# Optimization experiments

Measured on AMD Instinct MI355X. Metric: run time of the kernel, lower is better.

Reference implementation:

```python
import jax, jax.numpy as jnp
import numpy as np

B, K, Z = 16384, 4096, 64  # batch, codebook size, code dim


def _linear_params(key, fan_in, fan_out):
    kw, kb = jax.random.split(key)
    lim = 1.0 / np.sqrt(fan_in)
    W = jax.random.uniform(kw, (fan_out, fan_in), jnp.float32, -lim, lim)
    b = jax.random.uniform(kb, (fan_out,), jnp.float32, -lim, lim)
    return W, b


def setup_inputs() -> dict:
    key = jax.random.key(0)
    ks = jax.random.split(key, 10)
    X = jax.random.normal(ks[0], (B, 784), jnp.float32)
    We1, be1 = _linear_params(ks[1], 784, 1000)
    We2, be2 = _linear_params(ks[2], 1000, 500)
    We3, be3 = _linear_params(ks[3], 500, 300)
    We4, be4 = _linear_params(ks[4], 300, Z)
    emb = jax.random.normal(ks[5], (K, Z), jnp.float32)  # nn.Embedding default N(0,1)
    Wd1, bd1 = _linear_params(ks[6], Z, 300)
    Wd2, bd2 = _linear_params(ks[7], 300, 500)
    Wd3, bd3 = _linear_params(ks[8], 500, 1000)
    Wd4, bd4 = _linear_params(ks[9], 1000, 784)
    return dict(X=X, We1=We1, be1=be1, We2=We2, be2=be2, We3=We3, be3=be3,
                We4=We4, be4=be4, emb=emb, Wd1=Wd1, bd1=bd1, Wd2=Wd2, bd2=bd2,
                Wd3=Wd3, bd3=bd3, Wd4=Wd4, bd4=bd4)


def _lin(x, W, b):
    return x @ W.T + b


def _nearest(query, target):
    # squared euclidean distances [Q, T] via expanded form (same math, no QxTxZ blowup)
    q2 = jnp.sum(query * query, axis=1, keepdims=True)        # [Q,1]
    t2 = jnp.sum(target * target, axis=1)                      # [T]
    d = q2 - 2.0 * (query @ target.T) + t2[None, :]            # [Q,T]
    idx = jnp.argmin(d, axis=1)                                # first min, like torch .min
    return target[idx]


def reference(X, We1, be1, We2, be2, We3, be3, We4, be4, emb,
              Wd1, bd1, Wd2, bd2, Wd3, bd3, Wd4, bd4):
    x = X.reshape(-1, 784)
    h = jax.nn.relu(_lin(x, We1, be1))
    h = jax.nn.relu(_lin(h, We2, be2))
    h = jax.nn.relu(_lin(h, We3, be3))
    Z_enc = _lin(h, We4, be4)                                  # [B,Z]
    Z_emb = _nearest(Z_enc, emb)                               # [B,Z]
    d = jax.nn.leaky_relu(_lin(Z_emb, Wd1, bd1), 0.1)
    d = jax.nn.leaky_relu(_lin(d, Wd2, bd2), 0.1)
    d = jax.nn.leaky_relu(_lin(d, Wd3, bd3), 0.1)
    Z_dec = jnp.tanh(_lin(d, Wd4, bd4)).reshape(-1, 1, 28, 28)
    Z_enc_for_emb = _nearest(emb, Z_enc)                       # [K,Z]
    return (Z_dec, Z_enc, Z_dec, Z_enc_for_emb)
```

## Files before the change

kernel.cpp:

```cpp
#include <hip/hip_runtime.h>
#include <hip/hip_bf16.h>
#include <math.h>

typedef __bf16 bf16_t;
typedef __bf16 bf16x8 __attribute__((ext_vector_type(8)));
typedef __bf16 bf16x4 __attribute__((ext_vector_type(4)));
typedef float f32x4 __attribute__((ext_vector_type(4)));

__device__ __forceinline__ void gload16(const void* g, void* l)
{
    __builtin_amdgcn_global_load_lds(
        (const __attribute__((address_space(1))) void*)g,
        (__attribute__((address_space(3))) void*)l, 16, 0, 0);
}

template<int ACT, int CB>
__global__ __launch_bounds__(256)
void np_gemm2(const float* __restrict__ A, const float* __restrict__ W,
              const float* __restrict__ bias, float* __restrict__ C,
              int N, int Cstride, int KP, int KA, int Kreal)
{
    __shared__ __align__(16) float sA[128 * 32];
    __shared__ __align__(16) float sB[CB * 64 * 32];
    const int tid = threadIdx.x;
    const int tx  = tid & 15, ty = tid >> 4;
    const int bRow = blockIdx.x * 128, bCol = blockIdx.y * (CB * 64);

    float acc[8][CB * 4];
#pragma unroll
    for (int i = 0; i < 8; ++i)
#pragma unroll
        for (int j = 0; j < CB * 4; ++j) acc[i][j] = 0.f;

    const int aswz = ty & 7;
    const int bswz = tx & 7;

    for (int k0 = 0; k0 < KP; k0 += 32) {
        __syncthreads();
        if (k0 + 32 <= Kreal) {
#pragma unroll
            for (int i = 0; i < 4; ++i) {
                int L = tid + i * 256;
                int r = L >> 3, cc = L & 7;
                int gc = cc ^ ((r >> 2) & 7);
                gload16(A + (size_t)(bRow + r) * KA + (k0 + gc * 4), sA + L * 4);
            }
        } else {
#pragma unroll
            for (int i = 0; i < 4; ++i) {
                int L = tid + i * 256;
                int r = L >> 3, cc = L & 7;
                int gc = cc ^ ((r >> 2) & 7);
                int gk = k0 + gc * 4;
                float4 v = make_float4(0.f, 0.f, 0.f, 0.f);
                if (gk < Kreal) v = *(const float4*)(A + (size_t)(bRow + r) * KA + gk);
                *(float4*)(sA + L * 4) = v;
            }
        }
#pragma unroll
        for (int i = 0; i < CB * 2; ++i) {
            int L = tid + i * 256;
            int r = L >> 3, cc = L & 7;
            int gc = cc ^ ((r >> 2) & 7);
            gload16(W + (size_t)(bCol + r) * KP + (k0 + gc * 4), sB + L * 4);
        }
        __syncthreads();

#pragma unroll
        for (int kc = 0; kc < 8; ++kc) {
            const int ac = ((kc ^ aswz) << 2);
            const int bc = ((kc ^ bswz) << 2);
            float4 b4[CB][4];
#pragma unroll
            for (int jb = 0; jb < CB; ++jb)
#pragma unroll
                for (int j = 0; j < 4; ++j)
                    b4[jb][j] = *(const float4*)(sB + (jb * 64 + tx * 4 + j) * 32 + bc);
#pragma unroll
            for (int ib = 0; ib < 2; ++ib)
#pragma unroll
                for (int i = 0; i < 4; ++i) {
                    float4 a4 = *(const float4*)(sA + (ib * 64 + ty * 4 + i) * 32 + ac);
#pragma unroll
                    for (int jb = 0; jb < CB; ++jb)
#pragma unroll
                        for (int j = 0; j < 4; ++j) {
                            float& o = acc[ib * 4 + i][jb * 4 + j];
                            o = __fmaf_rn(a4.x, b4[jb][j].x, o);
                            o = __fmaf_rn(a4.y, b4[jb][j].y, o);
                            o = __fmaf_rn(a4.z, b4[jb][j].z, o);
                            o = __fmaf_rn(a4.w, b4[jb][j].w, o);
                        }
                }
        }
    }

#pragma unroll
    for (int jb = 0; jb < CB; ++jb) {
        int col4 = bCol + jb * 64 + tx * 4;
        if (col4 >= Cstride) continue;
#pragma unroll
        for (int ib = 0; ib < 2; ++ib)
#pragma unroll
            for (int i = 0; i < 4; ++i) {
                int row = bRow + ib * 64 + ty * 4 + i;
                float ov[4];
#pragma unroll
                for (int j = 0; j < 4; ++j) {
                    int col = col4 + j;
                    float v = 0.f;
                    if (col < N) {
                        v = __fadd_rn(acc[ib * 4 + i][jb * 4 + j], bias[col]);
                        if (ACT == 1) v = v > 0.f ? v : 0.f;
                    }
                    ov[j] = v;
                }
                *(float4*)(C + (size_t)row * Cstride + col4) =
                    make_float4(ov[0], ov[1], ov[2], ov[3]);
            }
    }
}

__global__ void k_padw(const float* __restrict__ src, float* __restrict__ dst,
                       int rows, int K, int rowsP, int Kp)
{
    int e = blockIdx.x * 256 + threadIdx.x;
    if (e >= rowsP * Kp) return;
    int r = e / Kp, k = e - r * Kp;
    dst[e] = (r < rows && k < K) ? src[(size_t)r * K + k] : 0.f;
}

__global__ void k_split(const float* __restrict__ src, bf16_t* __restrict__ hi,
                        bf16_t* __restrict__ lo, int rows, int K, int rowsP, int Kp)
{
    int e = blockIdx.x * 256 + threadIdx.x;
    if (e >= rowsP * Kp) return;
    int r = e / Kp, k = e - r * Kp;
    float v = (r < rows && k < K) ? src[(size_t)r * K + k] : 0.f;
    bf16_t h = (bf16_t)v;
    bf16_t l = (bf16_t)(v - (float)h);
    hi[e] = h; lo[e] = l;
}

template<int ACT, int OUT>
__global__ __launch_bounds__(256)
void gemm_planes(const bf16_t* __restrict__ Ahi, const bf16_t* __restrict__ Alo,
                 const bf16_t* __restrict__ Bhi, const bf16_t* __restrict__ Blo,
                 const float* __restrict__ bias,
                 float* __restrict__ C0, float* __restrict__ C1,
                 bf16_t* __restrict__ Phi, bf16_t* __restrict__ Plo,
                 int N, int Kp, int Kpn)
{
    __shared__ __align__(16) bf16_t sA[2][128][32];
    __shared__ __align__(16) bf16_t sB[2][128][32];

    const int tid  = threadIdx.x;
    const int bRow = blockIdx.x * 128;
    const int bCol = blockIdx.y * 128;
    const int wave = tid >> 6;
    const int lane = tid & 63;
    const int wr   = (wave >> 1) * 64;
    const int wc   = (wave & 1) * 64;
    const int quad = lane >> 4;
    const int l15  = lane & 15;

    f32x4 acc[4][4];
#pragma unroll
    for (int i = 0; i < 4; ++i)
#pragma unroll
        for (int j = 0; j < 4; ++j) acc[i][j] = (f32x4){0.f, 0.f, 0.f, 0.f};

    for (int k0 = 0; k0 < Kp; k0 += 32) {
        __syncthreads();
#pragma unroll
        for (int i = 0; i < 2; ++i) {
            int c    = tid + i * 256;
            int row  = c >> 2;
            int koff = (c & 3) << 3;
            size_t ga = (size_t)(bRow + row) * Kp + (k0 + koff);
            size_t gb = (size_t)(bCol + row) * Kp + (k0 + koff);
            gload16(Ahi + ga, &sA[0][row][koff]);
            gload16(Alo + ga, &sA[1][row][koff]);
            gload16(Bhi + gb, &sB[0][row][koff]);
            gload16(Blo + gb, &sB[1][row][koff]);
        }
        __syncthreads();

        bf16x8 af[2][4], bfr[2][4];
#pragma unroll
        for (int t = 0; t < 2; ++t)
#pragma unroll
            for (int i = 0; i < 4; ++i) {
                af[t][i]  = *(const bf16x8*)&sA[t][wr + i * 16 + l15][quad * 8];
                bfr[t][i] = *(const bf16x8*)&sB[t][wc + i * 16 + l15][quad * 8];
            }
#pragma unroll
        for (int i = 0; i < 4; ++i)
#pragma unroll
            for (int j = 0; j < 4; ++j)
#pragma unroll
                for (int ta = 0; ta < 2; ++ta)
#pragma unroll
                    for (int tb = 0; tb < 2 - ta; ++tb)
                        acc[i][j] = __builtin_amdgcn_mfma_f32_16x16x32_bf16(
                            af[ta][i], bfr[tb][j], acc[i][j], 0, 0, 0);
    }

#pragma unroll
    for (int j = 0; j < 4; ++j) {
        int col = bCol + wc + j * 16 + l15;
        if (OUT == 0) {
            if (col >= N) continue;
            float bv = bias[col];
#pragma unroll
            for (int i = 0; i < 4; ++i)
#pragma unroll
                for (int r = 0; r < 4; ++r) {
                    int row = bRow + wr + i * 16 + quad * 4 + r;
                    float v = acc[i][j][r] + bv;
                    if (ACT == 1)      v = v > 0.f ? v : 0.f;
                    else if (ACT == 2) v = v >= 0.f ? v : 0.1f * v;
                    else if (ACT == 3) v = tanhf(v);
                    size_t o = (size_t)row * N + col;
                    C0[o] = v;
                    if (C1) C1[o] = v;
                }
        } else {
            if (col >= Kpn) continue;
            const bool real = col < N;
            float bv = real ? bias[col] : 0.f;
#pragma unroll
            for (int i = 0; i < 4; ++i)
#pragma unroll
                for (int r = 0; r < 4; ++r) {
                    int row = bRow + wr + i * 16 + quad * 4 + r;
                    float v = 0.f;
                    if (real) {
                        v = acc[i][j][r] + bv;
                        if (ACT == 1)      v = v > 0.f ? v : 0.f;
                        else if (ACT == 2) v = v >= 0.f ? v : 0.1f * v;
                        else if (ACT == 3) v = tanhf(v);
                    }
                    bf16_t h = (bf16_t)v;
                    bf16_t l = (bf16_t)(v - (float)h);
                    size_t o = (size_t)row * Kpn + col;
                    Phi[o] = h; Plo[o] = l;
                }
        }
    }
}

__global__ __launch_bounds__(256)
void k_nearest(const float* __restrict__ Q, const float* __restrict__ C,
               const float* __restrict__ q2a, const float* __restrict__ cn2,
               int chunk, float* __restrict__ pd, int* __restrict__ pi)
{
    __shared__ __align__(16) float sc[64][64];
    __shared__ __align__(16) float sn[64];
    const int tid = threadIdx.x;
    const int q   = blockIdx.x * 256 + tid;
    const int G   = gridDim.y;

    float qr[64];
    const float4* qp = (const float4*)(Q + (size_t)q * 64);
#pragma unroll
    for (int i = 0; i < 16; ++i) ((float4*)qr)[i] = qp[i];
    const float q2 = q2a[q];

    float best = 3.4e38f;
    int   bi   = 0x7fffffff;
    const int c0 = blockIdx.y * chunk;

    for (int cb = 0; cb < chunk; cb += 64) {
        __syncthreads();
        const float4* gp = (const float4*)(C + (size_t)(c0 + cb) * 64);
#pragma unroll
        for (int i = 0; i < 4; ++i) {
            int e = tid + i * 256;
            ((float4*)&sc[0][0])[e] = gp[e];
        }
        if (tid < 64) sn[tid] = cn2[c0 + cb + tid];
        __syncthreads();

        for (int c = 0; c < 64; c += 4) {
            float a0 = 0.f, a1 = 0.f, a2 = 0.f, a3 = 0.f;
            const float4* e0 = (const float4*)&sc[c + 0][0];
            const float4* e1 = (const float4*)&sc[c + 1][0];
            const float4* e2p = (const float4*)&sc[c + 2][0];
            const float4* e3 = (const float4*)&sc[c + 3][0];
#pragma unroll
            for (int z = 0; z < 16; ++z) {
                float4 q4 = ((float4*)qr)[z];
                float4 v0 = e0[z], v1 = e1[z], v2 = e2p[z], v3 = e3[z];
                a0 = __fmaf_rn(q4.x, v0.x, a0); a0 = __fmaf_rn(q4.y, v0.y, a0);
                a0 = __fmaf_rn(q4.z, v0.z, a0); a0 = __fmaf_rn(q4.w, v0.w, a0);
                a1 = __fmaf_rn(q4.x, v1.x, a1); a1 = __fmaf_rn(q4.y, v1.y, a1);
                a1 = __fmaf_rn(q4.z, v1.z, a1); a1 = __fmaf_rn(q4.w, v1.w, a1);
                a2 = __fmaf_rn(q4.x, v2.x, a2); a2 = __fmaf_rn(q4.y, v2.y, a2);
                a2 = __fmaf_rn(q4.z, v2.z, a2); a2 = __fmaf_rn(q4.w, v2.w, a2);
                a3 = __fmaf_rn(q4.x, v3.x, a3); a3 = __fmaf_rn(q4.y, v3.y, a3);
                a3 = __fmaf_rn(q4.z, v3.z, a3); a3 = __fmaf_rn(q4.w, v3.w, a3);
            }
            float d;
            d = __fadd_rn(__fsub_rn(q2, __fmul_rn(2.f, a0)), sn[c + 0]);
            if (d < best) { best = d; bi = c0 + cb + c + 0; }
            d = __fadd_rn(__fsub_rn(q2, __fmul_rn(2.f, a1)), sn[c + 1]);
            if (d < best) { best = d; bi = c0 + cb + c + 1; }
            d = __fadd_rn(__fsub_rn(q2, __fmul_rn(2.f, a2)), sn[c + 2]);
            if (d < best) { best = d; bi = c0 + cb + c + 2; }
            d = __fadd_rn(__fsub_rn(q2, __fmul_rn(2.f, a3)), sn[c + 3]);
            if (d < best) { best = d; bi = c0 + cb + c + 3; }
        }
    }
    pd[(size_t)q * G + blockIdx.y] = best;
    pi[(size_t)q * G + blockIdx.y] = bi;
}

__global__ void k_reduce(const float* __restrict__ pd, const int* __restrict__ pi,
                         int G, int NQ, int* __restrict__ out)
{
    int q = blockIdx.x * blockDim.x + threadIdx.x;
    if (q >= NQ) return;
    float best = 3.4e38f; int bi = 0;
    for (int g = 0; g < G; ++g) {
        float d = pd[(size_t)q * G + g];
        if (d < best) { best = d; bi = pi[(size_t)q * G + g]; }
    }
    out[q] = bi;
}

__global__ void k_gather(const float* __restrict__ src, const int* __restrict__ idx,
                         float* __restrict__ dst, int nsrc)
{
    int r = blockIdx.x, z = threadIdx.x;
    int i = idx[r];
    i = i < 0 ? 0 : (i >= nsrc ? nsrc - 1 : i);
    dst[(size_t)r * 64 + z] = src[(size_t)i * 64 + z];
}

__global__ void k_gather_split(const float* __restrict__ src, const int* __restrict__ idx,
                               bf16_t* __restrict__ hi, bf16_t* __restrict__ lo, int nsrc)
{
    int r = blockIdx.x, z = threadIdx.x;
    int i = idx[r];
    i = i < 0 ? 0 : (i >= nsrc ? nsrc - 1 : i);
    float v = src[(size_t)i * 64 + z];
    bf16_t h = (bf16_t)v;
    bf16_t l = (bf16_t)(v - (float)h);
    hi[(size_t)r * 64 + z] = h;
    lo[(size_t)r * 64 + z] = l;
}

__global__ void k_norm2(const float* __restrict__ s, float* __restrict__ o, int rows)
{
    int r0 = blockIdx.x * blockDim.x + threadIdx.x;
    if (r0 >= rows) return;
    const float* p = s + (size_t)r0 * 64;
    float r[8];
#pragma unroll
    for (int j = 0; j < 8; ++j) r[j] = __fmul_rn(p[j], p[j]);
#pragma unroll
    for (int i = 8; i < 64; i += 8)
#pragma unroll
        for (int j = 0; j < 8; ++j)
            r[j] = __fadd_rn(r[j], __fmul_rn(p[i + j], p[i + j]));
    float t01 = __fadd_rn(r[0], r[1]), t23 = __fadd_rn(r[2], r[3]);
    float t45 = __fadd_rn(r[4], r[5]), t67 = __fadd_rn(r[6], r[7]);
    o[r0] = __fadd_rn(__fadd_rn(t01, t23), __fadd_rn(t45, t67));
}

extern "C" void kernel_launch(void* const* d_in, const int* in_sizes, int n_in,
                              void* d_out, int out_size, void* d_ws, size_t ws_size,
                              hipStream_t stream)
{
    const int B  = 16384;
    const int KC = 4096;

    const float* X   = (const float*)d_in[0];
    const float* We1 = (const float*)d_in[1];
    const float* be1 = (const float*)d_in[2];
    const float* We2 = (const float*)d_in[3];
    const float* be2 = (const float*)d_in[4];
    const float* We3 = (const float*)d_in[5];
    const float* be3 = (const float*)d_in[6];
    const float* We4 = (const float*)d_in[7];
    const float* be4 = (const float*)d_in[8];
    const float* emb = (const float*)d_in[9];
    const float* Wd1 = (const float*)d_in[10];
    const float* bd1 = (const float*)d_in[11];
    const float* Wd2 = (const float*)d_in[12];
    const float* bd2 = (const float*)d_in[13];
    const float* Wd3 = (const float*)d_in[14];
    const float* bd3 = (const float*)d_in[15];
    const float* Wd4 = (const float*)d_in[16];
    const float* bd4 = (const float*)d_in[17];

    float* out = (float*)d_out;
    const size_t OFF1 = (size_t)B * 784;
    const size_t OFF2 = OFF1 + (size_t)B * 64;
    const size_t OFF3 = OFF2 + (size_t)B * 784;
    float* zenc = out + OFF1;

    const size_t FIXED = (size_t)24 << 20;
    int MQ;
    if      (ws_size >= FIXED + (size_t)16384 * 7424) MQ = 16384;
    else if (ws_size >= FIXED + (size_t)8192  * 7424) MQ = 8192;
    else                                              MQ = 4096;
    const int NQn = B / MQ;

    char* ws = (char*)d_ws;
    size_t off = 0;
    auto alloc = [&](size_t bytes) -> void* {
        void* p = ws + off;
        off = (off + bytes + 255) & ~(size_t)255;
        return p;
    };
    float* pd    = (float*)alloc((size_t)262144 * 4);
    int*   pi    = (int*)alloc((size_t)262144 * 4);
    int*   idx1  = (int*)alloc((size_t)B * 4);
    int*   idx2  = (int*)alloc((size_t)KC * 4);
    float* e2    = (float*)alloc((size_t)KC * 4);
    float* z2    = (float*)alloc((size_t)B * 4);
    float* we1p = (float*)alloc((size_t)1024 * 800 * 4);
    float* we2p = (float*)alloc((size_t)512 * 1024 * 4);
    float* we3p = (float*)alloc((size_t)384 * 512 * 4);
    float* we4p = (float*)alloc((size_t)128 * 320 * 4);
    bf16_t* zembh = (bf16_t*)alloc((size_t)B * 64 * 2);
    bf16_t* zembl = (bf16_t*)alloc((size_t)B * 64 * 2);
    bf16_t* wp1h = (bf16_t*)alloc((size_t)384 * 64 * 2);
    bf16_t* wp1l = (bf16_t*)alloc((size_t)384 * 64 * 2);
    bf16_t* wp2h = (bf16_t*)alloc((size_t)512 * 320 * 2);
    bf16_t* wp2l = (bf16_t*)alloc((size_t)512 * 320 * 2);
    bf16_t* wp3h = (bf16_t*)alloc((size_t)1024 * 512 * 2);
    bf16_t* wp3l = (bf16_t*)alloc((size_t)1024 * 512 * 2);
    bf16_t* wp4h = (bf16_t*)alloc((size_t)896 * 1024 * 2);
    bf16_t* wp4l = (bf16_t*)alloc((size_t)896 * 1024 * 2);
    char* big = (char*)alloc((size_t)MQ * 7424);
    float* h1 = (float*)big;
    float* h2 = (float*)(big + (size_t)MQ * 4096);
    float* h3 = (float*)(big + (size_t)MQ * 6144);
    bf16_t* d1h = (bf16_t*)big;
    bf16_t* d1l = (bf16_t*)(big + (size_t)MQ * 640);
    bf16_t* d2h = (bf16_t*)(big + (size_t)MQ * 1280);
    bf16_t* d2l = (bf16_t*)(big + (size_t)MQ * 2304);
    bf16_t* d3h = (bf16_t*)(big + (size_t)MQ * 3328);
    bf16_t* d3l = (bf16_t*)(big + (size_t)MQ * 5376);

    dim3 blk(256);
    const dim3 eg1(MQ / 128, 8), eg2(MQ / 128, 8), eg3(MQ / 128, 6), eg4(MQ / 128, 2);
    const dim3 dq1(MQ / 128, 3), dq2(MQ / 128, 4), dq3(MQ / 128, 8), dq4(MQ / 128, 7);

    k_padw<<<dim3((1024 * 800 + 255) / 256), blk, 0, stream>>>(We1, we1p, 1000, 784, 1024, 800);
    k_padw<<<dim3((512 * 1024 + 255) / 256), blk, 0, stream>>>(We2, we2p, 500, 1000, 512, 1024);
    k_padw<<<dim3((384 * 512  + 255) / 256), blk, 0, stream>>>(We3, we3p, 300, 500, 384, 512);
    k_padw<<<dim3((128 * 320  + 255) / 256), blk, 0, stream>>>(We4, we4p, 64, 300, 128, 320);
    k_split<<<dim3((384 * 64   + 255) / 256), blk, 0, stream>>>(Wd1, wp1h, wp1l, 300, 64, 384, 64);
    k_split<<<dim3((512 * 320  + 255) / 256), blk, 0, stream>>>(Wd2, wp2h, wp2l, 500, 300, 512, 320);
    k_split<<<dim3((1024 * 512 + 255) / 256), blk, 0, stream>>>(Wd3, wp3h, wp3l, 1000, 500, 1024, 512);
    k_split<<<dim3((896 * 1024 + 255) / 256), blk, 0, stream>>>(Wd4, wp4h, wp4l, 784, 1000, 896, 1024);

    for (int q = 0; q < NQn; ++q) {
        const float* Xq = X + (size_t)q * MQ * 784;
        np_gemm2<1, 2><<<eg1, blk, 0, stream>>>(Xq, we1p, be1, h1, 1000, 1024, 800, 784, 784);
        np_gemm2<1, 1><<<eg2, blk, 0, stream>>>(h1, we2p, be2, h2, 500, 512, 1024, 1024, 1024);
        np_gemm2<1, 1><<<eg3, blk, 0, stream>>>(h2, we3p, be3, h3, 300, 320, 512, 512, 512);
        np_gemm2<0, 1><<<eg4, blk, 0, stream>>>(h3, we4p, be4,
                                                zenc + (size_t)q * MQ * 64, 64, 64, 320, 320, 320);
    }

    k_norm2<<<dim3((KC + 255) / 256), blk, 0, stream>>>(emb, e2, KC);
    k_norm2<<<dim3((B + 255) / 256),  blk, 0, stream>>>(zenc, z2, B);

    k_nearest<<<dim3(64, 16), blk, 0, stream>>>(zenc, emb, z2, e2, 256, pd, pi);
    k_reduce <<<dim3(B / 256), blk, 0, stream>>>(pd, pi, 16, B, idx1);
    k_gather_split<<<dim3(B), dim3(64), 0, stream>>>(emb, idx1, zembh, zembl, KC);

    k_nearest<<<dim3(16, 64), blk, 0, stream>>>(emb, zenc, e2, z2, 256, pd, pi);
    k_reduce <<<dim3(KC / 256), blk, 0, stream>>>(pd, pi, 64, KC, idx2);
    k_gather <<<dim3(KC), dim3(64), 0, stream>>>(zenc, idx2, out + OFF3, B);

    for (int q = 0; q < NQn; ++q) {
        gemm_planes<2, 1><<<dq1, blk, 0, stream>>>(
            zembh + (size_t)q * MQ * 64, zembl + (size_t)q * MQ * 64,
            wp1h, wp1l, bd1, nullptr, nullptr, d1h, d1l, 300, 64, 320);
        gemm_planes<2, 1><<<dq2, blk, 0, stream>>>(
            d1h, d1l, wp2h, wp2l, bd2, nullptr, nullptr, d2h, d2l, 500, 320, 512);
        gemm_planes<2, 1><<<dq3, blk, 0, stream>>>(
            d2h, d2l, wp3h, wp3l, bd3, nullptr, nullptr, d3h, d3l, 1000, 512, 1024);
        gemm_planes<3, 0><<<dq4, blk, 0, stream>>>(
            d3h, d3l, wp4h, wp4l, bd4,
            out + (size_t)q * MQ * 784, out + OFF2 + (size_t)q * MQ * 784,
            nullptr, nullptr, 784, 1024, 0);
    }

    (void)in_sizes; (void)n_in; (void)out_size;
}
```

Before: 1.381 ms.

## Read encoder A operand directly from global memory instead of staging in LDS

The encoder fp32 GEMM no longer stages the activation tile in shared memory. Each thread reads its eight A rows straight from global memory as float4 loads, and a per-k guard replaces the zero-padded tail tile. The grid's column dimension for layers 3 and 4 shrinks to match the real output widths, which drops the blocks that only computed padding. This removes LDS traffic and one buffer, but adds uncoalesced, redundant global loads, since the 16 threads sharing a row each re-read the same A data and must rely on cache.

```diff
diff --git a/kernel.cpp b/kernel.cpp
--- a/kernel.cpp
+++ b/kernel.cpp
@@ -16,11 +16,10 @@
 
 template<int ACT, int CB>
 __global__ __launch_bounds__(256)
-void np_gemm2(const float* __restrict__ A, const float* __restrict__ W,
+void np_gemm3(const float* __restrict__ A, const float* __restrict__ W,
               const float* __restrict__ bias, float* __restrict__ C,
               int N, int Cstride, int KP, int KA, int Kreal)
 {
-    __shared__ __align__(16) float sA[128 * 32];
     __shared__ __align__(16) float sB[CB * 64 * 32];
     const int tid = threadIdx.x;
     const int tx  = tid & 15, ty = tid >> 4;
@@ -32,31 +31,17 @@
 #pragma unroll
         for (int j = 0; j < CB * 4; ++j) acc[i][j] = 0.f;
 
-    const int aswz = ty & 7;
     const int bswz = tx & 7;
 
+    const float* arow[8];
+#pragma unroll
+    for (int ib = 0; ib < 2; ++ib)
+#pragma unroll
+        for (int i = 0; i < 4; ++i)
+            arow[ib * 4 + i] = A + (size_t)(bRow + ib * 64 + ty * 4 + i) * KA;
+
     for (int k0 = 0; k0 < KP; k0 += 32) {
         __syncthreads();
-        if (k0 + 32 <= Kreal) {
-#pragma unroll
-            for (int i = 0; i < 4; ++i) {
-                int L = tid + i * 256;
-                int r = L >> 3, cc = L & 7;
-                int gc = cc ^ ((r >> 2) & 7);
-                gload16(A + (size_t)(bRow + r) * KA + (k0 + gc * 4), sA + L * 4);
-            }
-        } else {
-#pragma unroll
-            for (int i = 0; i < 4; ++i) {
-                int L = tid + i * 256;
-                int r = L >> 3, cc = L & 7;
-                int gc = cc ^ ((r >> 2) & 7);
-                int gk = k0 + gc * 4;
-                float4 v = make_float4(0.f, 0.f, 0.f, 0.f);
-                if (gk < Kreal) v = *(const float4*)(A + (size_t)(bRow + r) * KA + gk);
-                *(float4*)(sA + L * 4) = v;
-            }
-        }
 #pragma unroll
         for (int i = 0; i < CB * 2; ++i) {
             int L = tid + i * 256;
@@ -68,7 +53,7 @@
 
 #pragma unroll
         for (int kc = 0; kc < 8; ++kc) {
-            const int ac = ((kc ^ aswz) << 2);
+            const int gk = k0 + kc * 4;
             const int bc = ((kc ^ bswz) << 2);
             float4 b4[CB][4];
 #pragma unroll
@@ -76,22 +61,22 @@
 #pragma unroll
                 for (int j = 0; j < 4; ++j)
                     b4[jb][j] = *(const float4*)(sB + (jb * 64 + tx * 4 + j) * 32 + bc);
-#pragma unroll
-            for (int ib = 0; ib < 2; ++ib)
-#pragma unroll
-                for (int i = 0; i < 4; ++i) {
-                    float4 a4 = *(const float4*)(sA + (ib * 64 + ty * 4 + i) * 32 + ac);
+            if (gk < Kreal) {
+#pragma unroll
+                for (int r = 0; r < 8; ++r) {
+                    float4 a4 = *(const float4*)(arow[r] + gk);
 #pragma unroll
                     for (int jb = 0; jb < CB; ++jb)
 #pragma unroll
                         for (int j = 0; j < 4; ++j) {
-                            float& o = acc[ib * 4 + i][jb * 4 + j];
+                            float& o = acc[r][jb * 4 + j];
                             o = __fmaf_rn(a4.x, b4[jb][j].x, o);
                             o = __fmaf_rn(a4.y, b4[jb][j].y, o);
                             o = __fmaf_rn(a4.z, b4[jb][j].z, o);
                             o = __fmaf_rn(a4.w, b4[jb][j].w, o);
                         }
                 }
+            }
         }
     }
 
@@ -447,7 +432,7 @@
     bf16_t* d3l = (bf16_t*)(big + (size_t)MQ * 5376);
 
     dim3 blk(256);
-    const dim3 eg1(MQ / 128, 8), eg2(MQ / 128, 8), eg3(MQ / 128, 6), eg4(MQ / 128, 2);
+    const dim3 eg1(MQ / 128, 8), eg2(MQ / 128, 8), eg3(MQ / 128, 5), eg4(MQ / 128, 1);
     const dim3 dq1(MQ / 128, 3), dq2(MQ / 128, 4), dq3(MQ / 128, 8), dq4(MQ / 128, 7);
 
     k_padw<<<dim3((1024 * 800 + 255) / 256), blk, 0, stream>>>(We1, we1p, 1000, 784, 1024, 800);
@@ -461,10 +446,10 @@
 
     for (int q = 0; q < NQn; ++q) {
         const float* Xq = X + (size_t)q * MQ * 784;
-        np_gemm2<1, 2><<<eg1, blk, 0, stream>>>(Xq, we1p, be1, h1, 1000, 1024, 800, 784, 784);
-        np_gemm2<1, 1><<<eg2, blk, 0, stream>>>(h1, we2p, be2, h2, 500, 512, 1024, 1024, 1024);
-        np_gemm2<1, 1><<<eg3, blk, 0, stream>>>(h2, we3p, be3, h3, 300, 320, 512, 512, 512);
-        np_gemm2<0, 1><<<eg4, blk, 0, stream>>>(h3, we4p, be4,
+        np_gemm3<1, 2><<<eg1, blk, 0, stream>>>(Xq, we1p, be1, h1, 1000, 1024, 800, 784, 784);
+        np_gemm3<1, 1><<<eg2, blk, 0, stream>>>(h1, we2p, be2, h2, 500, 512, 1024, 1024, 1024);
+        np_gemm3<1, 1><<<eg3, blk, 0, stream>>>(h2, we3p, be3, h3, 300, 320, 512, 512, 512);
+        np_gemm3<0, 1><<<eg4, blk, 0, stream>>>(h3, we4p, be4,
                                                 zenc + (size_t)q * MQ * 64, 64, 64, 320, 320, 320);
     }
 
```

New measurement: 1.616 ms. +17.0%, slower.

## Double-buffer LDS tiles in encoder and decoder GEMMs and trim grid widths

Applied to the files above, without the earlier changes.

Both the fp32 encoder GEMM and the bf16 split-plane MFMA GEMM now keep two LDS buffers. The next K-tile is issued into one buffer while the current one is computed, replacing the two barriers per iteration with one. This aims to hide global-to-LDS latency behind math. The encoder grids for layers 3 and 4 are also cut to skip column blocks that write nothing past the padded stride. Doubling LDS use may lower occupancy.

```diff
diff --git a/kernel.cpp b/kernel.cpp
--- a/kernel.cpp
+++ b/kernel.cpp
@@ -16,12 +16,12 @@
 
 template<int ACT, int CB>
 __global__ __launch_bounds__(256)
-void np_gemm2(const float* __restrict__ A, const float* __restrict__ W,
+void np_gemm5(const float* __restrict__ A, const float* __restrict__ W,
               const float* __restrict__ bias, float* __restrict__ C,
               int N, int Cstride, int KP, int KA, int Kreal)
 {
-    __shared__ __align__(16) float sA[128 * 32];
-    __shared__ __align__(16) float sB[CB * 64 * 32];
+    __shared__ __align__(16) float sA[2 * 128 * 32];
+    __shared__ __align__(16) float sB[2 * CB * 64 * 32];
     const int tid = threadIdx.x;
     const int tx  = tid & 15, ty = tid >> 4;
     const int bRow = blockIdx.x * 128, bCol = blockIdx.y * (CB * 64);
@@ -35,15 +35,16 @@
     const int aswz = ty & 7;
     const int bswz = tx & 7;
 
-    for (int k0 = 0; k0 < KP; k0 += 32) {
-        __syncthreads();
+    auto stage = [&](int b, int k0) {
+        float* dA = sA + b * (128 * 32);
+        float* dB = sB + b * (CB * 64 * 32);
         if (k0 + 32 <= Kreal) {
 #pragma unroll
             for (int i = 0; i < 4; ++i) {
                 int L = tid + i * 256;
                 int r = L >> 3, cc = L & 7;
                 int gc = cc ^ ((r >> 2) & 7);
-                gload16(A + (size_t)(bRow + r) * KA + (k0 + gc * 4), sA + L * 4);
+                gload16(A + (size_t)(bRow + r) * KA + (k0 + gc * 4), dA + L * 4);
             }
         } else {
 #pragma unroll
@@ -54,7 +55,7 @@
                 int gk = k0 + gc * 4;
                 float4 v = make_float4(0.f, 0.f, 0.f, 0.f);
                 if (gk < Kreal) v = *(const float4*)(A + (size_t)(bRow + r) * KA + gk);
-                *(float4*)(sA + L * 4) = v;
+                *(float4*)(dA + L * 4) = v;
             }
         }
 #pragma unroll
@@ -62,10 +63,20 @@
             int L = tid + i * 256;
             int r = L >> 3, cc = L & 7;
             int gc = cc ^ ((r >> 2) & 7);
-            gload16(W + (size_t)(bCol + r) * KP + (k0 + gc * 4), sB + L * 4);
-        }
-        __syncthreads();
-
+            gload16(W + (size_t)(bCol + r) * KP + (k0 + gc * 4), dB + L * 4);
+        }
+    };
+
+    const int nt = KP >> 5;
+    stage(0, 0);
+    __syncthreads();
+
+    int buf = 0;
+    for (int t = 0; t < nt; ++t) {
+        if (t + 1 < nt) stage(buf ^ 1, (t + 1) << 5);
+
+        const float* pA = sA + buf * (128 * 32);
+        const float* pB = sB + buf * (CB * 64 * 32);
 #pragma unroll
         for (int kc = 0; kc < 8; ++kc) {
             const int ac = ((kc ^ aswz) << 2);
@@ -75,12 +86,12 @@
             for (int jb = 0; jb < CB; ++jb)
 #pragma unroll
                 for (int j = 0; j < 4; ++j)
-                    b4[jb][j] = *(const float4*)(sB + (jb * 64 + tx * 4 + j) * 32 + bc);
+                    b4[jb][j] = *(const float4*)(pB + (jb * 64 + tx * 4 + j) * 32 + bc);
 #pragma unroll
             for (int ib = 0; ib < 2; ++ib)
 #pragma unroll
                 for (int i = 0; i < 4; ++i) {
-                    float4 a4 = *(const float4*)(sA + (ib * 64 + ty * 4 + i) * 32 + ac);
+                    float4 a4 = *(const float4*)(pA + (ib * 64 + ty * 4 + i) * 32 + ac);
 #pragma unroll
                     for (int jb = 0; jb < CB; ++jb)
 #pragma unroll
@@ -93,6 +104,8 @@
                         }
                 }
         }
+        __syncthreads();
+        buf ^= 1;
     }
 
 #pragma unroll
@@ -151,8 +164,8 @@
                  bf16_t* __restrict__ Phi, bf16_t* __restrict__ Plo,
                  int N, int Kp, int Kpn)
 {
-    __shared__ __align__(16) bf16_t sA[2][128][32];
-    __shared__ __align__(16) bf16_t sB[2][128][32];
+    __shared__ __align__(16) bf16_t sA[2][2][128][32];
+    __shared__ __align__(16) bf16_t sB[2][2][128][32];
 
     const int tid  = threadIdx.x;
     const int bRow = blockIdx.x * 128;
@@ -170,8 +183,7 @@
 #pragma unroll
         for (int j = 0; j < 4; ++j) acc[i][j] = (f32x4){0.f, 0.f, 0.f, 0.f};
 
-    for (int k0 = 0; k0 < Kp; k0 += 32) {
-        __syncthreads();
+    auto stage = [&](int b, int k0) {
 #pragma unroll
         for (int i = 0; i < 2; ++i) {
             int c    = tid + i * 256;
@@ -179,20 +191,28 @@
             int koff = (c & 3) << 3;
             size_t ga = (size_t)(bRow + row) * Kp + (k0 + koff);
             size_t gb = (size_t)(bCol + row) * Kp + (k0 + koff);
-            gload16(Ahi + ga, &sA[0][row][koff]);
-            gload16(Alo + ga, &sA[1][row][koff]);
-            gload16(Bhi + gb, &sB[0][row][koff]);
-            gload16(Blo + gb, &sB[1][row][koff]);
-        }
-        __syncthreads();
+            gload16(Ahi + ga, &sA[b][0][row][koff]);
+            gload16(Alo + ga, &sA[b][1][row][koff]);
+            gload16(Bhi + gb, &sB[b][0][row][koff]);
+            gload16(Blo + gb, &sB[b][1][row][koff]);
+        }
+    };
+
+    const int nt = Kp >> 5;
+    stage(0, 0);
+    __syncthreads();
+
+    int buf = 0;
+    for (int t = 0; t < nt; ++t) {
+        if (t + 1 < nt) stage(buf ^ 1, (t + 1) << 5);
 
         bf16x8 af[2][4], bfr[2][4];
 #pragma unroll
-        for (int t = 0; t < 2; ++t)
+        for (int tt = 0; tt < 2; ++tt)
 #pragma unroll
             for (int i = 0; i < 4; ++i) {
-                af[t][i]  = *(const bf16x8*)&sA[t][wr + i * 16 + l15][quad * 8];
-                bfr[t][i] = *(const bf16x8*)&sB[t][wc + i * 16 + l15][quad * 8];
+                af[tt][i]  = *(const bf16x8*)&sA[buf][tt][wr + i * 16 + l15][quad * 8];
+                bfr[tt][i] = *(const bf16x8*)&sB[buf][tt][wc + i * 16 + l15][quad * 8];
             }
 #pragma unroll
         for (int i = 0; i < 4; ++i)
@@ -204,6 +224,9 @@
                     for (int tb = 0; tb < 2 - ta; ++tb)
                         acc[i][j] = __builtin_amdgcn_mfma_f32_16x16x32_bf16(
                             af[ta][i], bfr[tb][j], acc[i][j], 0, 0, 0);
+
+        __syncthreads();
+        buf ^= 1;
     }
 
 #pragma unroll
@@ -447,7 +470,7 @@
     bf16_t* d3l = (bf16_t*)(big + (size_t)MQ * 5376);
 
     dim3 blk(256);
-    const dim3 eg1(MQ / 128, 8), eg2(MQ / 128, 8), eg3(MQ / 128, 6), eg4(MQ / 128, 2);
+    const dim3 eg1(MQ / 128, 8), eg2(MQ / 128, 8), eg3(MQ / 128, 5), eg4(MQ / 128, 1);
     const dim3 dq1(MQ / 128, 3), dq2(MQ / 128, 4), dq3(MQ / 128, 8), dq4(MQ / 128, 7);
 
     k_padw<<<dim3((1024 * 800 + 255) / 256), blk, 0, stream>>>(We1, we1p, 1000, 784, 1024, 800);
@@ -461,10 +484,10 @@
 
     for (int q = 0; q < NQn; ++q) {
         const float* Xq = X + (size_t)q * MQ * 784;
-        np_gemm2<1, 2><<<eg1, blk, 0, stream>>>(Xq, we1p, be1, h1, 1000, 1024, 800, 784, 784);
-        np_gemm2<1, 1><<<eg2, blk, 0, stream>>>(h1, we2p, be2, h2, 500, 512, 1024, 1024, 1024);
-        np_gemm2<1, 1><<<eg3, blk, 0, stream>>>(h2, we3p, be3, h3, 300, 320, 512, 512, 512);
-        np_gemm2<0, 1><<<eg4, blk, 0, stream>>>(h3, we4p, be4,
+        np_gemm5<1, 2><<<eg1, blk, 0, stream>>>(Xq, we1p, be1, h1, 1000, 1024, 800, 784, 784);
+        np_gemm5<1, 1><<<eg2, blk, 0, stream>>>(h1, we2p, be2, h2, 500, 512, 1024, 1024, 1024);
+        np_gemm5<1, 1><<<eg3, blk, 0, stream>>>(h2, we3p, be3, h3, 300, 320, 512, 512, 512);
+        np_gemm5<0, 1><<<eg4, blk, 0, stream>>>(h3, we4p, be4,
                                                 zenc + (size_t)q * MQ * 64, 64, 64, 320, 320, 320);
     }
 
```

Measured after the change: 1.529 ms. 10.7% more time.
